# Kernel tuning notes

Hardware: AMD Instinct MI355X
Metric: run time of the kernel (lower is better)

The kernel has to match this reference:

```python
import jax, jax.numpy as jnp
import numpy as np

N_NODES = 100000
N_EDGES = 1600000
D_FEAT = 32


def setup_inputs() -> dict:
    key = jax.random.key(0)
    k1, k2, k3, k4, k5 = jax.random.split(key, 5)
    src_feats = jax.random.normal(k1, (N_NODES, D_FEAT), dtype=jnp.float32)
    cj = jax.random.uniform(k2, (N_NODES, 1), dtype=jnp.float32)
    ci = jax.random.uniform(k3, (N_NODES, 1), dtype=jnp.float32)
    src_idx = jax.random.randint(k4, (N_EDGES,), 0, N_NODES, dtype=jnp.int32)
    dst_idx = jax.random.randint(k5, (N_EDGES,), 0, N_NODES, dtype=jnp.int32)
    return {"src_feats": src_feats, "cj": cj, "ci": ci,
            "src_idx": src_idx, "dst_idx": dst_idx}


def reference(src_feats, cj, ci, src_idx, dst_idx):
    # Dropout in eval mode (identity). Training-mode dropout is stochastic and
    # excluded from the correctness baseline.
    weighted = src_feats * cj                      # [N, d] scale by src norm coeff
    msgs = weighted[src_idx]                       # [E, d] gather (copy_u)
    agg = jax.ops.segment_sum(msgs, dst_idx, num_segments=N_NODES)  # [N, d] sum aggregate
    return agg * ci                                # [N, d] scale by dst norm coeff
```

## Files before the change

### kernel.cpp

```cpp
#include <hip/hip_runtime.h>

#define N_NODES 100000
#define N_EDGES 1600000
#define D_FEAT 32
#define CAP 32
#define NXCD 8
#define NODES_PER_XCD (N_NODES / NXCD)
#define EDGE_THREADS (N_EDGES / 4)
#define EDGE_BLOCKS ((EDGE_THREADS + 255) / 256)

typedef int   __attribute__((ext_vector_type(4))) i32x4;
typedef float __attribute__((ext_vector_type(4))) f32x4;

__global__ __launch_bounds__(256) void lgc_weight(
    const f32x4* __restrict__ feats4,
    const float* __restrict__ cj,
    f32x4*       __restrict__ w4)
{
    int tid = blockIdx.x * 256 + threadIdx.x;
    float c = cj[tid >> 3];
    f32x4 v = __builtin_nontemporal_load(&feats4[tid]);
    w4[tid] = v * c;
}

__global__ __launch_bounds__(256) void lgc_bucket(
    const i32x4* __restrict__ dst4,
    const i32x4* __restrict__ src4,
    const float* __restrict__ weighted,
    int*         __restrict__ cnt,
    int*         __restrict__ bucket,
    float*       __restrict__ out)
{
    int x  = blockIdx.x % NXCD;
    int lb = blockIdx.x / NXCD;
    int t  = lb * 256 + threadIdx.x;
    if (t >= EDGE_THREADS) return;

    const int lo = x * NODES_PER_XCD;
    const int hi = lo + NODES_PER_XCD;

    i32x4 d4 = __builtin_nontemporal_load(&dst4[t]);
    bool ix = (d4.x >= lo) & (d4.x < hi);
    bool iy = (d4.y >= lo) & (d4.y < hi);
    bool iz = (d4.z >= lo) & (d4.z < hi);
    bool iw = (d4.w >= lo) & (d4.w < hi);
    if (!(ix | iy | iz | iw)) return;

    i32x4 s4 = __builtin_nontemporal_load(&src4[t]);
    int ds[4] = {d4.x, d4.y, d4.z, d4.w};
    int ss[4] = {s4.x, s4.y, s4.z, s4.w};
    bool in[4] = {ix, iy, iz, iw};

    #pragma unroll
    for (int k = 0; k < 4; ++k) {
        if (!in[k]) continue;
        int d = ds[k], s = ss[k];
        int pos = atomicAdd(&cnt[d], 1);
        if (pos < CAP) {
            bucket[(size_t)d * CAP + pos] = s;
        } else {
            const float* row = weighted + (size_t)s * D_FEAT;
            float* o = out + (size_t)d * D_FEAT;
            for (int f = 0; f < D_FEAT; ++f) atomicAdd(o + f, row[f]);
        }
    }
}

__global__ __launch_bounds__(256) void lgc_gather(
    const f32x4* __restrict__ w4,
    const float* __restrict__ ci,
    const int*   __restrict__ cnt,
    const i32x4* __restrict__ bucket4,
    f32x4*       __restrict__ out4)
{
    int tid = blockIdx.x * 256 + threadIdx.x;
    int n = tid >> 3;
    int f = tid & 7;

    int c = cnt[n];
    if (c > CAP) c = CAP;
    const i32x4* b4 = bucket4 + (size_t)n * (CAP / 4);

    i32x4 r[8];
    #pragma unroll
    for (int j = 0; j < 8; ++j)
        if (j * 4 < c) r[j] = __builtin_nontemporal_load(&b4[j]);

    f32x4 acc = (f32x4)(0.f);
    #pragma unroll
    for (int j = 0; j < 8; ++j) {
        int base = j * 4;
        if (base < c) {
            i32x4 bv = r[j];
            acc += w4[(size_t)bv.x * 8 + f];
            if (base + 1 < c) acc += w4[(size_t)bv.y * 8 + f];
            if (base + 2 < c) acc += w4[(size_t)bv.z * 8 + f];
            if (base + 3 < c) acc += w4[(size_t)bv.w * 8 + f];
        }
    }

    float s = ci[n];
    f32x4 o = __builtin_nontemporal_load(&out4[tid]);
    __builtin_nontemporal_store((acc + o) * s, &out4[tid]);
}

__global__ __launch_bounds__(256) void lgc_scatter(
    const float4* __restrict__ src_feats4,
    const float*  __restrict__ cj,
    const int*    __restrict__ src_idx,
    const int*    __restrict__ dst_idx,
    float*        __restrict__ out)
{
    long tid = (long)blockIdx.x * blockDim.x + threadIdx.x;
    const long total = (long)N_EDGES * 8;
    if (tid >= total) return;
    int e  = (int)(tid >> 3);
    int f4 = (int)(tid & 7);
    int s = src_idx[e];
    int d = dst_idx[e];
    float c = cj[s];
    float4 v = src_feats4[s * 8 + f4];
    float* o = out + (size_t)d * D_FEAT + f4 * 4;
    atomicAdd(o + 0, v.x * c);
    atomicAdd(o + 1, v.y * c);
    atomicAdd(o + 2, v.z * c);
    atomicAdd(o + 3, v.w * c);
}

__global__ __launch_bounds__(256) void lgc_scale(
    float4*       __restrict__ out4,
    const float*  __restrict__ ci)
{
    int tid = blockIdx.x * blockDim.x + threadIdx.x;
    const int total = N_NODES * 8;
    if (tid >= total) return;
    float c = ci[tid >> 3];
    float4 v = out4[tid];
    v.x *= c; v.y *= c; v.z *= c; v.w *= c;
    out4[tid] = v;
}

extern "C" void kernel_launch(void* const* d_in, const int* in_sizes, int n_in,
                              void* d_out, int out_size, void* d_ws, size_t ws_size,
                              hipStream_t stream) {
    const float* src_feats = (const float*)d_in[0];
    const float* cj        = (const float*)d_in[1];
    const float* ci        = (const float*)d_in[2];
    const int*   src_idx   = (const int*)d_in[3];
    const int*   dst_idx   = (const int*)d_in[4];
    float*       out       = (float*)d_out;

    const size_t cnt_ints    = 102400;
    const size_t bucket_ints = (size_t)N_NODES * CAP;
    const size_t wfeat_flts  = (size_t)N_NODES * D_FEAT;
    const size_t need = (cnt_ints + bucket_ints + wfeat_flts) * 4;

    if (ws_size >= need) {
        int*   cnt      = (int*)d_ws;
        int*   bucket   = cnt + cnt_ints;
        float* weighted = (float*)(bucket + bucket_ints);

        hipMemsetAsync(cnt, 0, N_NODES * sizeof(int), stream);
        hipMemsetAsync(out, 0, (size_t)out_size * sizeof(float), stream);

        lgc_weight<<<(N_NODES * 8) / 256, 256, 0, stream>>>(
            (const f32x4*)src_feats, cj, (f32x4*)weighted);

        lgc_bucket<<<NXCD * EDGE_BLOCKS, 256, 0, stream>>>(
            (const i32x4*)dst_idx, (const i32x4*)src_idx, weighted,
            cnt, bucket, out);

        lgc_gather<<<(N_NODES * 8) / 256, 256, 0, stream>>>(
            (const f32x4*)weighted, ci, cnt, (const i32x4*)bucket, (f32x4*)out);
    } else {
        hipMemsetAsync(out, 0, (size_t)out_size * sizeof(float), stream);
        {
            const long total = (long)N_EDGES * 8;
            const int grid = (int)((total + 255) / 256);
            lgc_scatter<<<grid, 256, 0, stream>>>((const float4*)src_feats, cj,
                                                  src_idx, dst_idx, out);
        }
        {
            const int grid = (N_NODES * 8 + 255) / 256;
            lgc_scale<<<grid, 256, 0, stream>>>((float4*)out, ci);
        }
    }
}
```

Measured before the change: 187.8 us.

## Store weighted features as fp16 split tables and gather in two half passes

The pre-scaled feature table is now stored in fp16 and split into two 16-column tables (low and high halves). The gather runs twice, once per half, so each pass works on a table of about 3.2 MB that is more likely to stay in cache. This cuts the bytes moved per random row gather. The cost is that bucket indices and counts are read twice, and fp16 rounding lowers accuracy, which could break tolerance checks.

```diff
diff --git a/kernel.cpp b/kernel.cpp
--- a/kernel.cpp
+++ b/kernel.cpp
@@ -1,4 +1,5 @@
 #include <hip/hip_runtime.h>
+#include <hip/hip_fp16.h>
 
 #define N_NODES 100000
 #define N_EDGES 1600000
@@ -11,25 +12,46 @@
 
 typedef int   __attribute__((ext_vector_type(4))) i32x4;
 typedef float __attribute__((ext_vector_type(4))) f32x4;
+typedef unsigned __attribute__((ext_vector_type(2))) u32x2;
 
 __global__ __launch_bounds__(256) void lgc_weight(
     const f32x4* __restrict__ feats4,
     const float* __restrict__ cj,
-    f32x4*       __restrict__ w4)
+    u32x2*       __restrict__ wlo,
+    u32x2*       __restrict__ whi)
 {
     int tid = blockIdx.x * 256 + threadIdx.x;
-    float c = cj[tid >> 3];
+    int n = tid >> 3, f4 = tid & 7;
+    float c = cj[n];
     f32x4 v = __builtin_nontemporal_load(&feats4[tid]);
-    w4[tid] = v * c;
+    __half2 h0 = __floats2half2_rn(v.x * c, v.y * c);
+    __half2 h1 = __floats2half2_rn(v.z * c, v.w * c);
+    u32x2 u;
+    u.x = *(const unsigned*)&h0;
+    u.y = *(const unsigned*)&h1;
+    u32x2* base = (f4 < 4) ? wlo : whi;
+    base[(size_t)n * 4 + (f4 & 3)] = u;
+}
+
+__device__ __forceinline__ void spill_row(const __half* __restrict__ wlo,
+                                          const __half* __restrict__ whi,
+                                          float* __restrict__ out, int s, int d)
+{
+    float* o = out + (size_t)d * D_FEAT;
+    for (int f = 0; f < 16; ++f)
+        atomicAdd(o + f,      __half2float(wlo[(size_t)s * 16 + f]));
+    for (int f = 0; f < 16; ++f)
+        atomicAdd(o + 16 + f, __half2float(whi[(size_t)s * 16 + f]));
 }
 
 __global__ __launch_bounds__(256) void lgc_bucket(
-    const i32x4* __restrict__ dst4,
-    const i32x4* __restrict__ src4,
-    const float* __restrict__ weighted,
-    int*         __restrict__ cnt,
-    int*         __restrict__ bucket,
-    float*       __restrict__ out)
+    const i32x4*  __restrict__ dst4,
+    const i32x4*  __restrict__ src4,
+    const __half* __restrict__ wlo,
+    const __half* __restrict__ whi,
+    int*          __restrict__ cnt,
+    int*          __restrict__ bucket,
+    float*        __restrict__ out)
 {
     int x  = blockIdx.x % NXCD;
     int lb = blockIdx.x / NXCD;
@@ -59,23 +81,22 @@
         if (pos < CAP) {
             bucket[(size_t)d * CAP + pos] = s;
         } else {
-            const float* row = weighted + (size_t)s * D_FEAT;
-            float* o = out + (size_t)d * D_FEAT;
-            for (int f = 0; f < D_FEAT; ++f) atomicAdd(o + f, row[f]);
+            spill_row(wlo, whi, out, s, d);
         }
     }
 }
 
-__global__ __launch_bounds__(256) void lgc_gather(
-    const f32x4* __restrict__ w4,
+__global__ __launch_bounds__(256) void lgc_gather_half(
+    const u32x2* __restrict__ w,
     const float* __restrict__ ci,
     const int*   __restrict__ cnt,
     const i32x4* __restrict__ bucket4,
-    f32x4*       __restrict__ out4)
+    f32x4*       __restrict__ outh)
 {
     int tid = blockIdx.x * 256 + threadIdx.x;
-    int n = tid >> 3;
-    int f = tid & 7;
+    if (tid >= N_NODES * 4) return;
+    int n = tid >> 2;
+    int q = tid & 3;
 
     int c = cnt[n];
     if (c > CAP) c = CAP;
@@ -86,22 +107,38 @@
     for (int j = 0; j < 8; ++j)
         if (j * 4 < c) r[j] = __builtin_nontemporal_load(&b4[j]);
 
-    f32x4 acc = (f32x4)(0.f);
+    float a0 = 0.f, a1 = 0.f, a2 = 0.f, a3 = 0.f;
+    auto row = [&](int s) {
+        u32x2 u = w[(size_t)s * 4 + q];
+        unsigned ux = u.x, uy = u.y;
+        __half2 p0 = *(__half2*)&ux;
+        __half2 p1 = *(__half2*)&uy;
+        float2 f0 = __half22float2(p0);
+        float2 f1 = __half22float2(p1);
+        a0 += f0.x; a1 += f0.y; a2 += f1.x; a3 += f1.y;
+    };
+
     #pragma unroll
     for (int j = 0; j < 8; ++j) {
         int base = j * 4;
         if (base < c) {
             i32x4 bv = r[j];
-            acc += w4[(size_t)bv.x * 8 + f];
-            if (base + 1 < c) acc += w4[(size_t)bv.y * 8 + f];
-            if (base + 2 < c) acc += w4[(size_t)bv.z * 8 + f];
-            if (base + 3 < c) acc += w4[(size_t)bv.w * 8 + f];
+            row(bv.x);
+            if (base + 1 < c) row(bv.y);
+            if (base + 2 < c) row(bv.z);
+            if (base + 3 < c) row(bv.w);
         }
     }
 
-    float s = ci[n];
-    f32x4 o = __builtin_nontemporal_load(&out4[tid]);
-    __builtin_nontemporal_store((acc + o) * s, &out4[tid]);
+    float sc = ci[n];
+    f32x4* op = outh + (size_t)n * 8 + q;
+    f32x4 o = __builtin_nontemporal_load(op);
+    f32x4 res;
+    res.x = (a0 + o.x) * sc;
+    res.y = (a1 + o.y) * sc;
+    res.z = (a2 + o.z) * sc;
+    res.w = (a3 + o.w) * sc;
+    __builtin_nontemporal_store(res, op);
 }
 
 __global__ __launch_bounds__(256) void lgc_scatter(
@@ -152,26 +189,32 @@
 
     const size_t cnt_ints    = 102400;
     const size_t bucket_ints = (size_t)N_NODES * CAP;
-    const size_t wfeat_flts  = (size_t)N_NODES * D_FEAT;
-    const size_t need = (cnt_ints + bucket_ints + wfeat_flts) * 4;
+    const size_t wtab_bytes  = (size_t)N_NODES * 16 * sizeof(__half);
+    const size_t need = (cnt_ints + bucket_ints) * 4 + 2 * wtab_bytes;
 
     if (ws_size >= need) {
-        int*   cnt      = (int*)d_ws;
-        int*   bucket   = cnt + cnt_ints;
-        float* weighted = (float*)(bucket + bucket_ints);
+        int*    cnt    = (int*)d_ws;
+        int*    bucket = cnt + cnt_ints;
+        __half* wlo    = (__half*)(bucket + bucket_ints);
+        __half* whi    = wlo + (size_t)N_NODES * 16;
 
         hipMemsetAsync(cnt, 0, N_NODES * sizeof(int), stream);
         hipMemsetAsync(out, 0, (size_t)out_size * sizeof(float), stream);
 
         lgc_weight<<<(N_NODES * 8) / 256, 256, 0, stream>>>(
-            (const f32x4*)src_feats, cj, (f32x4*)weighted);
+            (const f32x4*)src_feats, cj, (u32x2*)wlo, (u32x2*)whi);
 
         lgc_bucket<<<NXCD * EDGE_BLOCKS, 256, 0, stream>>>(
-            (const i32x4*)dst_idx, (const i32x4*)src_idx, weighted,
+            (const i32x4*)dst_idx, (const i32x4*)src_idx, wlo, whi,
             cnt, bucket, out);
 
-        lgc_gather<<<(N_NODES * 8) / 256, 256, 0, stream>>>(
-            (const f32x4*)weighted, ci, cnt, (const i32x4*)bucket, (f32x4*)out);
+        const int ggrid = (N_NODES * 4 + 255) / 256;
+        lgc_gather_half<<<ggrid, 256, 0, stream>>>(
+            (const u32x2*)wlo, ci, cnt, (const i32x4*)bucket,
+            (f32x4*)out + 0);
+        lgc_gather_half<<<ggrid, 256, 0, stream>>>(
+            (const u32x2*)whi, ci, cnt, (const i32x4*)bucket,
+            (f32x4*)out + 4);
     } else {
         hipMemsetAsync(out, 0, (size_t)out_size * sizeof(float), stream);
         {
```

After: 194.6 us. 3.6% more time.
